# Kernel optimization log

Hardware: AMD Instinct MI355X
Metric: run time of the kernel (lower is better)

## Reference

```python
import jax, jax.numpy as jnp
import numpy as np

S, B, IN, H, OUT = 128, 256, 1024, 1024, 1024

def setup_inputs() -> dict:
    key = jax.random.key(0)
    ks = jax.random.split(key, 10)
    sc_ih = 1.0 / np.sqrt(IN)
    sc_h = 1.0 / np.sqrt(H)
    return {
        "inputs": jax.random.normal(ks[0], (S, B, IN), dtype=jnp.float32),
        "h0": jax.random.normal(ks[1], (B, H), dtype=jnp.float32),
        "c0": jax.random.normal(ks[2], (B, H), dtype=jnp.float32),
        "W_ih": jax.random.normal(ks[3], (4 * H, IN), dtype=jnp.float32) * sc_ih,
        "W_hh": jax.random.normal(ks[4], (4 * H, H), dtype=jnp.float32) * sc_h,
        "b_ih": jax.random.normal(ks[5], (4 * H,), dtype=jnp.float32) * sc_h,
        "b_hh": jax.random.normal(ks[6], (4 * H,), dtype=jnp.float32) * sc_h,
        "attnW": jax.random.normal(ks[7], (S, S), dtype=jnp.float32),
        "linW": jax.random.normal(ks[8], (OUT, H), dtype=jnp.float32) * sc_h,
        "linb": jax.random.normal(ks[9], (OUT,), dtype=jnp.float32) * sc_h,
    }

def _lstm_scan(inputs, h0, c0, W_ih, W_hh, b_ih, b_hh):
    # PyTorch LSTM gate order: i, f, g, o
    def step(carry, x_t):
        h, c = carry
        gates = x_t @ W_ih.T + b_ih + h @ W_hh.T + b_hh  # [B, 4H]
        i, f, g, o = jnp.split(gates, 4, axis=-1)
        i = jax.nn.sigmoid(i)
        f = jax.nn.sigmoid(f)
        g = jnp.tanh(g)
        o = jax.nn.sigmoid(o)
        c = f * c + i * g
        h = o * jnp.tanh(c)
        return (h, c), h
    (_, _), hs = jax.lax.scan(step, (h0, c0), inputs)
    return hs  # [S, B, H]

def reference(inputs, h0, c0, W_ih, W_hh, b_ih, b_hh, attnW, linW, linb):
    hs = _lstm_scan(inputs, h0, c0, W_ih, W_hh, b_ih, b_hh)  # [S, B, H]
    A = jax.nn.softmax(attnW, axis=-1)  # F.softmax default on 2D -> dim=1
    att = jnp.einsum('xy,ybh->xbh', A, hs)  # weighted sum of hidden states
    out = att @ linW.T + linb  # [S, B, OUT]
    return out.reshape(-1, OUT)  # [S*B, OUT]
```

## Files before the change

### kernel.cpp

```cpp
#include <hip/hip_runtime.h>


typedef _Float16 half8 __attribute__((ext_vector_type(8)));
typedef float f32x4 __attribute__((ext_vector_type(4)));

#define S_  128
#define B_  256
#define HDIM 1024
#define BH  262144

__device__ __forceinline__ void g2l16(void* lds_base, const void* g) {
  __builtin_amdgcn_global_load_lds(
      (const __attribute__((address_space(1))) void*)g,
      (__attribute__((address_space(3))) void*)lds_base, 16, 0, 0);
}

__device__ __forceinline__ float sigmoidf_(float x) {
  return 1.f / (1.f + __expf(-x));
}
__device__ __forceinline__ float tanhf_(float x) {
  float e = __expf(-2.f * fabsf(x));
  float t = (1.f - e) / (1.f + e);
  return x < 0.f ? -t : t;
}

__global__ __launch_bounds__(256) void k_cvt(const float* __restrict__ src,
                                             _Float16* __restrict__ dst) {
  size_t i = ((size_t)blockIdx.x * 256 + threadIdx.x) * 8;
  float4 u = *(const float4*)(src + i);
  float4 v = *(const float4*)(src + i + 4);
  half8 h;
  h[0] = u.x; h[1] = u.y; h[2] = u.z; h[3] = u.w;
  h[4] = v.x; h[5] = v.y; h[6] = v.z; h[7] = v.w;
  *(half8*)(dst + i) = h;
}

__global__ __launch_bounds__(256) void k_wcat(const float* __restrict__ Wih,
                                              const float* __restrict__ Whh,
                                              _Float16* __restrict__ Wc) {
  size_t i = ((size_t)blockIdx.x * 256 + threadIdx.x) * 8;
  int r = (int)(i >> 11), k = (int)(i & 2047);
  const float* src = (k < 1024) ? (Wih + (size_t)r * 1024 + k)
                                : (Whh + (size_t)r * 1024 + (k - 1024));
  float4 u = *(const float4*)(src);
  float4 v = *(const float4*)(src + 4);
  half8 h;
  h[0] = u.x; h[1] = u.y; h[2] = u.z; h[3] = u.w;
  h[4] = v.x; h[5] = v.y; h[6] = v.z; h[7] = v.w;
  *(half8*)(Wc + i) = h;
}

__global__ __launch_bounds__(256) void k_init(const float* __restrict__ h0,
                                              const float* __restrict__ c0,
                                              const float* __restrict__ bih,
                                              const float* __restrict__ bhh,
                                              _Float16* __restrict__ hs0,
                                              float* __restrict__ cbuf,
                                              float* __restrict__ bias) {
  int i = blockIdx.x * 256 + threadIdx.x;
  cbuf[i] = c0[i];
  hs0[i] = (_Float16)h0[i];
  if (i < 4096) bias[i] = bih[i] + bhh[i];
}

__global__ __launch_bounds__(64) void k_softmax(const float* __restrict__ W,
                                                _Float16* __restrict__ Ah,
                                                _Float16* __restrict__ Ar) {
  int r = blockIdx.x, lane = threadIdx.x;
  float v0 = W[r * 128 + lane], v1 = W[r * 128 + 64 + lane];
  float m = fmaxf(v0, v1);
  for (int off = 32; off; off >>= 1) m = fmaxf(m, __shfl_xor(m, off));
  float e0 = __expf(v0 - m), e1 = __expf(v1 - m);
  float s = e0 + e1;
  for (int off = 32; off; off >>= 1) s += __shfl_xor(s, off);
  float inv = 1.f / s;
  float a0 = e0 * inv, a1 = e1 * inv;
  _Float16 h0 = (_Float16)a0, h1 = (_Float16)a1;
  Ah[r * 128 + lane] = h0;
  Ah[r * 128 + 64 + lane] = h1;
  Ar[r * 128 + lane] = (_Float16)(a0 - (float)h0);
  Ar[r * 128 + 64 + lane] = (_Float16)(a1 - (float)h1);
}

__global__ __launch_bounds__(512) void k_step(const _Float16* __restrict__ Xh,
                                              const _Float16* __restrict__ Wc,
                                              const float* __restrict__ bias,
                                              _Float16* __restrict__ hs,
                                              float* __restrict__ cbuf,
                                              int t) {
  __shared__ char smem[131072];
  const int tid = threadIdx.x;
  const int wid = tid >> 6;
  const int lane = tid & 63;
  const int kg = wid >> 2;
  const int wv = wid & 3;
  const int tg = tid & 255;
  const int n_tile = blockIdx.x & 63;
  const int m_tile = blockIdx.x >> 6;
  const int n0 = n_tile * 16;
  const int m0 = m_tile * 64;

  const _Float16* Asrc = (kg == 0) ? (Xh + (size_t)t * BH)
                                   : (hs + (size_t)t * BH);
  const int kbase = kg * 1024;

  f32x4 acc[4];
  #pragma unroll
  for (int g = 0; g < 4; ++g) acc[g] = (f32x4){0.f, 0.f, 0.f, 0.f};

  int offA[2], offB[2];
  #pragma unroll
  for (int q = 0; q < 4; ++q) {
    int s = q * 256 + tg;
    if (q < 2) {
      int r = s >> 3, c = s & 7;
      int kc = c ^ (r & 7);
      offA[q] = (m0 + r) * 1024 + kc * 8;
    } else {
      int sb = s - 512;
      int r = sb >> 3, c = sb & 7;
      int kc = c ^ (r & 7);
      int row = (r >> 4) * 1024 + n0 + (r & 15);
      offB[q - 2] = row * 2048 + kbase + kc * 8;
    }
  }

  char* gbase = smem + kg * 65536;
  auto stage = [&](int buf, int k0) {
    char* base = gbase + buf * 16384;
    #pragma unroll
    for (int q = 0; q < 4; ++q) {
      char* dst = base + (q * 4 + wv) * 1024;
      if (q < 2) g2l16(dst, Asrc + offA[q] + k0);
      else       g2l16(dst, Wc + offB[q - 2] + k0);
    }
  };

  const int ra = wv * 16 + (lane & 15);
  const int kcl = lane >> 4;
  const int aoff0 = ra * 128 + ((kcl ^ (ra & 7)) * 16);
  const int aoff1 = ra * 128 + (((kcl + 4) ^ (ra & 7)) * 16);
  int boff0[4], boff1[4];
  #pragma unroll
  for (int g = 0; g < 4; ++g) {
    int rb = g * 16 + (lane & 15);
    boff0[g] = 8192 + rb * 128 + ((kcl ^ (rb & 7)) * 16);
    boff1[g] = 8192 + rb * 128 + (((kcl + 4) ^ (rb & 7)) * 16);
  }

  stage(0, 0);
  stage(1, 64);

  #pragma unroll
  for (int iter = 0; iter < 16; ++iter) {
    if (iter < 14) stage((iter + 2) & 3, (iter + 2) * 64);
    if (iter < 14)       asm volatile("s_waitcnt vmcnt(8)" ::: "memory");
    else if (iter == 14) asm volatile("s_waitcnt vmcnt(4)" ::: "memory");
    else                 asm volatile("s_waitcnt vmcnt(0)" ::: "memory");
    __builtin_amdgcn_s_barrier();
    const char* At = gbase + (iter & 3) * 16384;
    half8 a0 = *(const half8*)(At + aoff0);
    half8 a1 = *(const half8*)(At + aoff1);
    #pragma unroll
    for (int g = 0; g < 4; ++g) {
      half8 b0 = *(const half8*)(At + boff0[g]);
      acc[g] = __builtin_amdgcn_mfma_f32_16x16x32_f16(a0, b0, acc[g], 0, 0, 0);
    }
    #pragma unroll
    for (int g = 0; g < 4; ++g) {
      half8 b1 = *(const half8*)(At + boff1[g]);
      acc[g] = __builtin_amdgcn_mfma_f32_16x16x32_f16(a1, b1, acc[g], 0, 0, 0);
    }
  }

  __syncthreads();

  {
    float* EXg = (float*)smem + kg * 4224;
    #pragma unroll
    for (int g = 0; g < 4; ++g) {
      int gc = g * 16 + (lane & 15);
      int mb = wv * 16 + (lane >> 4) * 4;
      #pragma unroll
      for (int r = 0; r < 4; ++r)
        EXg[(mb + r) * 66 + gc] = acc[g][r];
    }
  }
  __syncthreads();

  {
    int nl = tid & 15;
    int mseg = tid >> 4;
    int n = n0 + nl;
    float bi = bias[n], bf2 = bias[1024 + n];
    float bg = bias[2048 + n], bo = bias[3072 + n];
    const float* E0 = (float*)smem;
    const float* E1 = E0 + 4224;
    _Float16* hnext = hs + (size_t)(t + 1) * BH;
    #pragma unroll
    for (int rr = 0; rr < 2; ++rr) {
      int m = mseg * 2 + rr;
      const float* e0 = E0 + m * 66;
      const float* e1 = E1 + m * 66;
      float gi = sigmoidf_(e0[nl]      + e1[nl]      + bi);
      float gf = sigmoidf_(e0[16 + nl] + e1[16 + nl] + bf2);
      float gg = tanhf_   (e0[32 + nl] + e1[32 + nl] + bg);
      float go = sigmoidf_(e0[48 + nl] + e1[48 + nl] + bo);
      size_t idx = (size_t)(m0 + m) * 1024 + n;
      float c = gf * cbuf[idx] + gi * gg;
      cbuf[idx] = c;
      hnext[idx] = (_Float16)(go * tanhf_(c));
    }
  }
}

__global__ __launch_bounds__(256) void k_attn(const _Float16* __restrict__ Ah,
                                              const _Float16* __restrict__ Ar,
                                              const _Float16* __restrict__ hs,
                                              _Float16* __restrict__ att) {
  __shared__ char smem[131072];
  const int tid = threadIdx.x;
  const int wave = tid >> 6;
  const int lane = tid & 63;
  const int n0 = blockIdx.x * 256;

  #pragma unroll
  for (int q = 0; q < 16; ++q) {
    int s = q * 256 + tid;
    char* dst = smem + (q * 4 + wave) * 1024;
    if (q < 8) {
      int r = s >> 4;
      int cl = (s & 15) ^ (r & 15);
      g2l16(dst, Ah + r * 128 + cl * 8);
    } else {
      int s2 = s - 2048;
      int r = s2 >> 4;
      int cl = (s2 & 15) ^ (r & 15);
      g2l16(dst, Ar + r * 128 + cl * 8);
    }
  }
  #pragma unroll
  for (int ch = 0; ch < 4; ++ch) {
    char* base = smem + 65536 + ch * 16384;
    #pragma unroll
    for (int q = 0; q < 4; ++q) {
      int s = q * 256 + tid;
      int y = s >> 5, cp = s & 31;
      int cl = cp ^ (((y >> 3) & 3) << 1);
      g2l16(base + (q * 4 + wave) * 1024,
            hs + (size_t)(1 + ch * 32 + y) * BH + n0 + cl * 8);
    }
  }

  f32x4 acc[8][4];
  #pragma unroll
  for (int m = 0; m < 8; ++m)
    #pragma unroll
    for (int nf = 0; nf < 4; ++nf) acc[m][nf] = (f32x4){0.f, 0.f, 0.f, 0.f};

  const int yg = lane >> 4;

  #pragma unroll
  for (int ch = 0; ch < 4; ++ch) {
    if (ch == 0)      asm volatile("s_waitcnt vmcnt(12)" ::: "memory");
    else if (ch == 1) asm volatile("s_waitcnt vmcnt(8)"  ::: "memory");
    else if (ch == 2) asm volatile("s_waitcnt vmcnt(4)"  ::: "memory");
    else              asm volatile("s_waitcnt vmcnt(0)"  ::: "memory");
    __builtin_amdgcn_s_barrier();

    const char* cb = smem + 65536 + ch * 16384;
    half8 b[4];
    #pragma unroll
    for (int nf = 0; nf < 4; ++nf) {
      int n = wave * 64 + nf * 16 + (lane & 15);
      const char* col = cb + (((n >> 3) ^ (yg << 1)) * 16) + (n & 7) * 2;
      #pragma unroll
      for (int j = 0; j < 8; ++j)
        b[nf][j] = *(const _Float16*)(col + (yg * 8 + j) * 512);
    }
    #pragma unroll
    for (int m = 0; m < 8; ++m) {
      int x = m * 16 + (lane & 15);
      int sw = ((ch * 4 + yg) ^ (x & 15)) * 16;
      half8 ah = *(const half8*)(smem + x * 256 + sw);
      half8 ar = *(const half8*)(smem + 32768 + x * 256 + sw);
      #pragma unroll
      for (int nf = 0; nf < 4; ++nf) {
        acc[m][nf] = __builtin_amdgcn_mfma_f32_16x16x32_f16(ah, b[nf], acc[m][nf], 0, 0, 0);
        acc[m][nf] = __builtin_amdgcn_mfma_f32_16x16x32_f16(ar, b[nf], acc[m][nf], 0, 0, 0);
      }
    }
  }

  #pragma unroll
  for (int m = 0; m < 8; ++m) {
    int x0 = m * 16 + (lane >> 4) * 4;
    #pragma unroll
    for (int nf = 0; nf < 4; ++nf) {
      int n = n0 + wave * 64 + nf * 16 + (lane & 15);
      #pragma unroll
      for (int r = 0; r < 4; ++r)
        att[(size_t)(x0 + r) * BH + n] = (_Float16)acc[m][nf][r];
    }
  }
}

__global__ __launch_bounds__(256) void k_final(const _Float16* __restrict__ att,
                                               const _Float16* __restrict__ Wl,
                                               const float* __restrict__ bvec,
                                               float* __restrict__ out) {
  __shared__ char smem[65536];
  const int tid = threadIdx.x, wave = tid >> 6, lane = tid & 63;
  const int j = blockIdx.x >> 3;
  const int m0 = (((blockIdx.x & 7) << 5) | (j >> 3)) * 128;
  const int n0 = (j & 7) * 128;
  const int mh = (wave & 1) * 64, nh = (wave >> 1) * 64;

  f32x4 acc[4][4];
  #pragma unroll
  for (int i = 0; i < 4; ++i)
    #pragma unroll
    for (int jj = 0; jj < 4; ++jj) acc[i][jj] = (f32x4){0.f, 0.f, 0.f, 0.f};

  auto stage = [&](int p, int k0) {
    char* base = smem + p * 32768;
    #pragma unroll
    for (int q = 0; q < 8; ++q) {
      int grp = q * 4 + wave;
      char* dst = base + grp * 1024;
      int s = grp * 64 + lane;
      if (s < 1024) {
        int r = s >> 3, c = s & 7;
        int kc = c ^ (r & 7);
        g2l16(dst, att + (size_t)(m0 + r) * 1024 + k0 + kc * 8);
      } else {
        int sb = s - 1024;
        int r = sb >> 3, c = sb & 7;
        int kc = c ^ (r & 7);
        g2l16(dst, Wl + (size_t)(n0 + r) * 1024 + k0 + kc * 8);
      }
    }
  };

  stage(0, 0);
  for (int iter = 0; iter < 16; ++iter) {
    int p = iter & 1;
    __syncthreads();
    if (iter + 1 < 16) stage(1 - p, (iter + 1) * 64);
    const char* At = smem + p * 32768;
    const char* Bt = At + 16384;
    #pragma unroll
    for (int k32 = 0; k32 < 2; ++k32) {
      int kc = k32 * 4 + (lane >> 4);
      half8 a[4], b[4];
      #pragma unroll
      for (int i = 0; i < 4; ++i) {
        int ra = mh + i * 16 + (lane & 15);
        a[i] = *(const half8*)(At + ra * 128 + ((kc ^ (ra & 7)) * 16));
        int rb = nh + i * 16 + (lane & 15);
        b[i] = *(const half8*)(Bt + rb * 128 + ((kc ^ (rb & 7)) * 16));
      }
      #pragma unroll
      for (int i = 0; i < 4; ++i)
        #pragma unroll
        for (int jj = 0; jj < 4; ++jj)
          acc[i][jj] = __builtin_amdgcn_mfma_f32_16x16x32_f16(a[i], b[jj], acc[i][jj], 0, 0, 0);
    }
  }

  #pragma unroll
  for (int i = 0; i < 4; ++i) {
    int m = m0 + mh + i * 16 + (lane >> 4) * 4;
    #pragma unroll
    for (int jj = 0; jj < 4; ++jj) {
      int n = n0 + nh + jj * 16 + (lane & 15);
      float bv = bvec[n];
      #pragma unroll
      for (int r = 0; r < 4; ++r)
        out[(size_t)(m + r) * 1024 + n] = acc[i][jj][r] + bv;
    }
  }
}

extern "C" void kernel_launch(void* const* d_in, const int* in_sizes, int n_in,
                              void* d_out, int out_size, void* d_ws, size_t ws_size,
                              hipStream_t stream) {
  const float* X     = (const float*)d_in[0];
  const float* h0    = (const float*)d_in[1];
  const float* c0    = (const float*)d_in[2];
  const float* Wih   = (const float*)d_in[3];
  const float* Whh   = (const float*)d_in[4];
  const float* bih   = (const float*)d_in[5];
  const float* bhh   = (const float*)d_in[6];
  const float* attnW = (const float*)d_in[7];
  const float* linW  = (const float*)d_in[8];
  const float* linb  = (const float*)d_in[9];
  float* out = (float*)d_out;
  char* ws = (char*)d_ws;

  _Float16* Xh  = (_Float16*)(ws + 0);
  _Float16* Wc  = (_Float16*)(ws + 67108864);
  _Float16* Wl  = (_Float16*)(ws + 83886080);
  _Float16* hs  = (_Float16*)(ws + 85983232);
  _Float16* att = (_Float16*)(ws + 153616384);
  float* cbuf   = (float*)(ws + 220725248);
  float* bias   = (float*)(ws + 221773824);
  _Float16* Ahm = (_Float16*)(ws + 221790208);
  _Float16* Arm = (_Float16*)(ws + 221822976);

  k_cvt<<<16384, 256, 0, stream>>>(X, Xh);
  k_wcat<<<4096, 256, 0, stream>>>(Wih, Whh, Wc);
  k_cvt<<<512, 256, 0, stream>>>(linW, Wl);
  k_init<<<1024, 256, 0, stream>>>(h0, c0, bih, bhh, hs, cbuf, bias);
  k_softmax<<<128, 64, 0, stream>>>(attnW, Ahm, Arm);

  for (int t = 0; t < S_; ++t)
    k_step<<<256, 512, 0, stream>>>(Xh, Wc, bias, hs, cbuf, t);

  k_attn<<<1024, 256, 0, stream>>>(Ahm, Arm, hs, att);
  k_final<<<2048, 256, 0, stream>>>(att, Wl, linb, out);
}
```

Baseline: 1.636 ms.

## Split LSTM step GEMM into four K-groups using 32x32x16 MFMA tiles

The per-timestep gate GEMM now splits K into four groups of two waves each instead of two groups of four waves. Each wave computes a 32x64 tile with 32x32x16 MFMA instructions rather than 16x16x32 ones. Staging chunks shrink to 32 columns with a 4-way XOR swizzle. The epilogue reduces four partial sums from LDS instead of two. The aim is fewer LDS fragment reads per MFMA and more K-parallelism, at the cost of a larger cross-wave reduction and lower LDS use per group.

```diff
diff --git a/kernel.cpp b/kernel.cpp
--- a/kernel.cpp
+++ b/kernel.cpp
@@ -3,6 +3,7 @@
 
 typedef _Float16 half8 __attribute__((ext_vector_type(8)));
 typedef float f32x4 __attribute__((ext_vector_type(4)));
+typedef float f32x16 __attribute__((ext_vector_type(16)));
 
 #define S_  128
 #define B_  256
@@ -90,100 +91,103 @@
                                               int t) {
   __shared__ char smem[131072];
   const int tid = threadIdx.x;
+  const int lane = tid & 63;
   const int wid = tid >> 6;
-  const int lane = tid & 63;
-  const int kg = wid >> 2;
-  const int wv = wid & 3;
-  const int tg = tid & 255;
+  const int kq = wid >> 1;
+  const int mh = wid & 1;
+  const int tg = tid & 127;
+  const int l31 = lane & 31;
+  const int lhi = lane >> 5;
   const int n_tile = blockIdx.x & 63;
   const int m_tile = blockIdx.x >> 6;
   const int n0 = n_tile * 16;
   const int m0 = m_tile * 64;
 
-  const _Float16* Asrc = (kg == 0) ? (Xh + (size_t)t * BH)
+  const _Float16* Abase = (kq < 2) ? (Xh + (size_t)t * BH)
                                    : (hs + (size_t)t * BH);
-  const int kbase = kg * 1024;
-
-  f32x4 acc[4];
-  #pragma unroll
-  for (int g = 0; g < 4; ++g) acc[g] = (f32x4){0.f, 0.f, 0.f, 0.f};
+  const int acolbase = (kq & 1) * 512;
+
+  f32x16 acc0 = {0.f};
+  f32x16 acc1 = {0.f};
 
   int offA[2], offB[2];
   #pragma unroll
-  for (int q = 0; q < 4; ++q) {
-    int s = q * 256 + tg;
-    if (q < 2) {
-      int r = s >> 3, c = s & 7;
-      int kc = c ^ (r & 7);
-      offA[q] = (m0 + r) * 1024 + kc * 8;
-    } else {
-      int sb = s - 512;
-      int r = sb >> 3, c = sb & 7;
-      int kc = c ^ (r & 7);
-      int row = (r >> 4) * 1024 + n0 + (r & 15);
-      offB[q - 2] = row * 2048 + kbase + kc * 8;
-    }
-  }
-
-  char* gbase = smem + kg * 65536;
-  auto stage = [&](int buf, int k0) {
-    char* base = gbase + buf * 16384;
-    #pragma unroll
-    for (int q = 0; q < 4; ++q) {
-      char* dst = base + (q * 4 + wv) * 1024;
-      if (q < 2) g2l16(dst, Asrc + offA[q] + k0);
-      else       g2l16(dst, Wc + offB[q - 2] + k0);
-    }
+  for (int q = 0; q < 2; ++q) {
+    int s = q * 128 + tg;
+    int r = s >> 2, c = s & 3;
+    int kc = c ^ (r & 3);
+    offA[q] = (m0 + r) * 1024 + kc * 8;
+  }
+  #pragma unroll
+  for (int q = 0; q < 2; ++q) {
+    int sb = q * 128 + tg;
+    int r = sb >> 2, c = sb & 3;
+    int kc = c ^ (r & 3);
+    int row = (r >> 4) * 1024 + n0 + (r & 15);
+    offB[q] = row * 2048 + kq * 512 + kc * 8;
+  }
+
+  char* gbase = smem + kq * 32768;
+  auto stage = [&](int buf, int it) {
+    char* base = gbase + buf * 8192;
+    int ka = acolbase + it * 32;
+    int kb = it * 32;
+    g2l16(base +        mh * 1024, Abase + offA[0] + ka);
+    g2l16(base + 2048 + mh * 1024, Abase + offA[1] + ka);
+    g2l16(base + 4096 + mh * 1024, Wc + offB[0] + kb);
+    g2l16(base + 6144 + mh * 1024, Wc + offB[1] + kb);
   };
 
-  const int ra = wv * 16 + (lane & 15);
-  const int kcl = lane >> 4;
-  const int aoff0 = ra * 128 + ((kcl ^ (ra & 7)) * 16);
-  const int aoff1 = ra * 128 + (((kcl + 4) ^ (ra & 7)) * 16);
-  int boff0[4], boff1[4];
-  #pragma unroll
-  for (int g = 0; g < 4; ++g) {
-    int rb = g * 16 + (lane & 15);
-    boff0[g] = 8192 + rb * 128 + ((kcl ^ (rb & 7)) * 16);
-    boff1[g] = 8192 + rb * 128 + (((kcl + 4) ^ (rb & 7)) * 16);
+  int aoff[2], boff[2][2];
+  #pragma unroll
+  for (int j = 0; j < 2; ++j) {
+    int ra = mh * 32 + l31;
+    int ca = j * 2 + lhi;
+    aoff[j] = ra * 64 + ((ca ^ (ra & 3)) * 16);
+    #pragma unroll
+    for (int f = 0; f < 2; ++f) {
+      int rb = f * 32 + l31;
+      int cb = j * 2 + lhi;
+      boff[f][j] = 4096 + rb * 64 + ((cb ^ (rb & 3)) * 16);
+    }
   }
 
   stage(0, 0);
-  stage(1, 64);
-
-  #pragma unroll
-  for (int iter = 0; iter < 16; ++iter) {
-    if (iter < 14) stage((iter + 2) & 3, (iter + 2) * 64);
-    if (iter < 14)       asm volatile("s_waitcnt vmcnt(8)" ::: "memory");
-    else if (iter == 14) asm volatile("s_waitcnt vmcnt(4)" ::: "memory");
-    else                 asm volatile("s_waitcnt vmcnt(0)" ::: "memory");
+  stage(1, 1);
+
+  #pragma unroll
+  for (int it = 0; it < 16; ++it) {
+    if (it < 14) stage((it + 2) & 3, it + 2);
+    if (it < 14)       asm volatile("s_waitcnt vmcnt(8)" ::: "memory");
+    else if (it == 14) asm volatile("s_waitcnt vmcnt(4)" ::: "memory");
+    else               asm volatile("s_waitcnt vmcnt(0)" ::: "memory");
     __builtin_amdgcn_s_barrier();
-    const char* At = gbase + (iter & 3) * 16384;
-    half8 a0 = *(const half8*)(At + aoff0);
-    half8 a1 = *(const half8*)(At + aoff1);
-    #pragma unroll
-    for (int g = 0; g < 4; ++g) {
-      half8 b0 = *(const half8*)(At + boff0[g]);
-      acc[g] = __builtin_amdgcn_mfma_f32_16x16x32_f16(a0, b0, acc[g], 0, 0, 0);
-    }
-    #pragma unroll
-    for (int g = 0; g < 4; ++g) {
-      half8 b1 = *(const half8*)(At + boff1[g]);
-      acc[g] = __builtin_amdgcn_mfma_f32_16x16x32_f16(a1, b1, acc[g], 0, 0, 0);
-    }
+    const char* bb = gbase + (it & 3) * 8192;
+    half8 a0 = *(const half8*)(bb + aoff[0]);
+    half8 b0 = *(const half8*)(bb + boff[0][0]);
+    half8 b1 = *(const half8*)(bb + boff[1][0]);
+    acc0 = __builtin_amdgcn_mfma_f32_32x32x16_f16(a0, b0, acc0, 0, 0, 0);
+    acc1 = __builtin_amdgcn_mfma_f32_32x32x16_f16(a0, b1, acc1, 0, 0, 0);
+    half8 a1 = *(const half8*)(bb + aoff[1]);
+    half8 b2 = *(const half8*)(bb + boff[0][1]);
+    half8 b3 = *(const half8*)(bb + boff[1][1]);
+    acc0 = __builtin_amdgcn_mfma_f32_32x32x16_f16(a1, b2, acc0, 0, 0, 0);
+    acc1 = __builtin_amdgcn_mfma_f32_32x32x16_f16(a1, b3, acc1, 0, 0, 0);
   }
 
   __syncthreads();
 
   {
-    float* EXg = (float*)smem + kg * 4224;
-    #pragma unroll
-    for (int g = 0; g < 4; ++g) {
-      int gc = g * 16 + (lane & 15);
-      int mb = wv * 16 + (lane >> 4) * 4;
-      #pragma unroll
-      for (int r = 0; r < 4; ++r)
-        EXg[(mb + r) * 66 + gc] = acc[g][r];
+    float* EXg = (float*)smem + kq * 4224 + mh * 32 * 66;
+    #pragma unroll
+    for (int f = 0; f < 2; ++f) {
+      const f32x16 a = f ? acc1 : acc0;
+      int gr = f * 32 + l31;
+      #pragma unroll
+      for (int e = 0; e < 16; ++e) {
+        int mr = (e & 3) + 8 * (e >> 2) + 4 * lhi;
+        EXg[mr * 66 + gr] = a[e];
+      }
     }
   }
   __syncthreads();
@@ -194,18 +198,16 @@
     int n = n0 + nl;
     float bi = bias[n], bf2 = bias[1024 + n];
     float bg = bias[2048 + n], bo = bias[3072 + n];
-    const float* E0 = (float*)smem;
-    const float* E1 = E0 + 4224;
+    const float* EX = (const float*)smem;
     _Float16* hnext = hs + (size_t)(t + 1) * BH;
     #pragma unroll
     for (int rr = 0; rr < 2; ++rr) {
       int m = mseg * 2 + rr;
-      const float* e0 = E0 + m * 66;
-      const float* e1 = E1 + m * 66;
-      float gi = sigmoidf_(e0[nl]      + e1[nl]      + bi);
-      float gf = sigmoidf_(e0[16 + nl] + e1[16 + nl] + bf2);
-      float gg = tanhf_   (e0[32 + nl] + e1[32 + nl] + bg);
-      float go = sigmoidf_(e0[48 + nl] + e1[48 + nl] + bo);
+      const float* e = EX + m * 66;
+      float gi = sigmoidf_(e[nl]      + e[4224 + nl]      + e[8448 + nl]      + e[12672 + nl]      + bi);
+      float gf = sigmoidf_(e[16 + nl] + e[4224 + 16 + nl] + e[8448 + 16 + nl] + e[12672 + 16 + nl] + bf2);
+      float gg = tanhf_   (e[32 + nl] + e[4224 + 32 + nl] + e[8448 + 32 + nl] + e[12672 + 32 + nl] + bg);
+      float go = sigmoidf_(e[48 + nl] + e[4224 + 48 + nl] + e[8448 + 48 + nl] + e[12672 + 48 + nl] + bo);
       size_t idx = (size_t)(m0 + m) * 1024 + n;
       float c = gf * cbuf[idx] + gi * gg;
       cbuf[idx] = c;
```

Result: slower. 2.151 ms (+31.5%).
